# Optimization experiments

Hardware: AMD Instinct MI355X
Metric: run time of the kernel (lower is better)

## Reference

```python
import jax, jax.numpy as jnp
import numpy as np

NUM_HEADS = 16


def setup_inputs() -> dict:
    key = jax.random.key(0)
    ks = jax.random.split(key, 4)
    B, T, D, H3 = 8, 1024, 1024, 3072
    Hd = 1024
    sequence = jax.random.normal(ks[0], (B, T, D), dtype=jnp.float32)
    mask = jnp.ones((B, T), dtype=jnp.int32)
    qkv_w = jax.random.normal(ks[1], (D, H3), dtype=jnp.float32) * (1.0 / np.sqrt(D))
    qkv_b = jnp.zeros((H3,), dtype=jnp.float32)
    out_w = jax.random.normal(ks[2], (Hd, Hd), dtype=jnp.float32) * (1.0 / np.sqrt(Hd))
    out_b = jnp.zeros((Hd,), dtype=jnp.float32)
    return {"sequence": sequence, "mask": mask, "qkv_w": qkv_w, "qkv_b": qkv_b,
            "out_w": out_w, "out_b": out_b}


def reference(sequence, mask, qkv_w, qkv_b, out_w, out_b):
    B, T, D = sequence.shape
    H = NUM_HEADS
    hidden = out_w.shape[0]
    hd = hidden // H
    scale = hd ** -0.5

    # qkv projection -> (3, B, H, T, hd)
    qkv = (sequence @ qkv_w + qkv_b).reshape(B, T, 3, H, hd).transpose(2, 0, 3, 1, 4)
    Q, K, V = qkv[0], qkv[1], qkv[2]

    attn = jnp.einsum('bhqd,bhkd->bhqk', Q, K) * scale
    # torch: masked_fill where mask.unsqueeze(1).unsqueeze(-1) == 0  -> masks query rows
    attn = jnp.where(mask[:, None, :, None] == 0, -jnp.inf, attn)
    attn_weights = jax.nn.softmax(attn, axis=-1)

    # global NaN fallback: if any NaN, replace entire tensor with one-hot at k=0
    has_nan = jnp.any(jnp.isnan(attn_weights))
    fallback = jnp.zeros_like(attn_weights).at[:, :, :, 0].set(1.0)
    attn_weights = jnp.where(has_nan, fallback, attn_weights)
    # dropout is identity in eval / p=0.0

    out = jnp.einsum('bhqk,bhkd->bhqd', attn_weights, V)
    out = out.transpose(0, 2, 1, 3).reshape(B, T, hidden)
    out = out @ out_w + out_b
    return out, attn_weights
```

## Files before the change

### kernel.cpp

```cpp
#include <hip/hip_runtime.h>
#include <hip/hip_bf16.h>

using u16 = unsigned short;
typedef short bf16x8 __attribute__((ext_vector_type(8)));
typedef float f32x4 __attribute__((ext_vector_type(4)));

#define MFMA16(a, b, c) __builtin_amdgcn_mfma_f32_16x16x32_bf16((a), (b), (c), 0, 0, 0)

__device__ __forceinline__ float bf2f(u16 u) {
  union { unsigned int i; float f; } v; v.i = ((unsigned int)u) << 16; return v.f;
}
__device__ __forceinline__ u16 f2bf(float f) {
  __hip_bfloat16 h = __float2bfloat16(f);
  return *reinterpret_cast<u16*>(&h);
}
__device__ __forceinline__ void gld_lds16(const void* g, void* l) {
  __builtin_amdgcn_global_load_lds(
      (const __attribute__((address_space(1))) void*)g,
      (__attribute__((address_space(3))) void*)l, 16, 0, 0);
}

__global__ __launch_bounds__(256) void cvt_f32_bf16(
    const float* __restrict__ in, u16* __restrict__ out, int n8) {
  int i = blockIdx.x * 256 + threadIdx.x;
  if (i >= n8) return;
  f32x4 a = *(const f32x4*)&in[(size_t)i * 8];
  f32x4 b = *(const f32x4*)&in[(size_t)i * 8 + 4];
  bf16x8 o;
#pragma unroll
  for (int j = 0; j < 4; ++j) { o[j] = (short)f2bf(a[j]); o[4 + j] = (short)f2bf(b[j]); }
  *(bf16x8*)&out[(size_t)i * 8] = o;
}

__global__ __launch_bounds__(256) void transpose_cvt(
    const float* __restrict__ in, u16* __restrict__ out, int R, int C) {
  __shared__ float tile[32][33];
  int r0 = blockIdx.y * 32, c0 = blockIdx.x * 32;
  int tx = threadIdx.x, ty = threadIdx.y;
#pragma unroll
  for (int i = ty; i < 32; i += 8)
    tile[i][tx] = in[(size_t)(r0 + i) * C + c0 + tx];
  __syncthreads();
#pragma unroll
  for (int i = ty; i < 32; i += 8)
    out[(size_t)(c0 + i) * R + r0 + tx] = f2bf(tile[tx][i]);
}

#define TBM 128
#define TBN 128
#define TBK 64
#define SLD 136

__global__ __launch_bounds__(256) void qkv_gemm(
    const u16* __restrict__ A, const u16* __restrict__ Bt,
    const float* __restrict__ bias,
    u16* __restrict__ Qo, u16* __restrict__ Ko, u16* __restrict__ Vto) {
  const int K = 1024;
  __shared__ __align__(16) u16 LDSbuf[TBM * SLD];
  u16* Als = LDSbuf;
  u16* Bls = LDSbuf + TBM * TBK;
  int m0 = blockIdx.y * TBM, n0 = blockIdx.x * TBN;
  int tid = threadIdx.x;
  int w = tid >> 6, l = tid & 63, lr = l & 15, lg = l >> 4;
  int wm = w >> 1, wn = w & 1;

  f32x4 acc[4][4] = {};
  for (int k0 = 0; k0 < K; k0 += TBK) {
#pragma unroll
    for (int j = 0; j < 4; ++j) {
      int c = w * 4 + j;
      int e = c * 64 + l;
      int row = e >> 3, kq = (e & 7) * 8;
      gld_lds16(A + (size_t)(m0 + row) * K + k0 + kq, (char*)Als + (size_t)c * 1024);
      gld_lds16(Bt + (size_t)(n0 + row) * K + k0 + kq, (char*)Bls + (size_t)c * 1024);
    }
    __syncthreads();
#pragma unroll
    for (int ks = 0; ks < 2; ++ks) {
      bf16x8 a[4], b[4];
#pragma unroll
      for (int mt = 0; mt < 4; ++mt)
        a[mt] = *(const bf16x8*)&Als[(wm * 64 + mt * 16 + lr) * TBK + ks * 32 + lg * 8];
#pragma unroll
      for (int nt = 0; nt < 4; ++nt)
        b[nt] = *(const bf16x8*)&Bls[(wn * 64 + nt * 16 + lr) * TBK + ks * 32 + lg * 8];
#pragma unroll
      for (int mt = 0; mt < 4; ++mt)
#pragma unroll
        for (int nt = 0; nt < 4; ++nt)
          acc[mt][nt] = MFMA16(a[mt], b[nt], acc[mt][nt]);
    }
    __syncthreads();
  }

  int s = n0 >> 10;
#pragma unroll
  for (int mt = 0; mt < 4; ++mt)
#pragma unroll
    for (int nt = 0; nt < 4; ++nt) {
      int nl = wn * 64 + nt * 16 + lr;
      float bv = bias[n0 + nl];
#pragma unroll
      for (int r = 0; r < 4; ++r) {
        int ml = wm * 64 + mt * 16 + lg * 4 + r;
        u16 val = f2bf(acc[mt][nt][r] + bv);
        if (s == 2) LDSbuf[nl * SLD + ml] = val;
        else        LDSbuf[ml * SLD + nl] = val;
      }
    }
  __syncthreads();

  int b_ = m0 >> 10;
  int tbase = m0 & 1023;
#pragma unroll
  for (int c = 0; c < 8; ++c) {
    int idx = c * 256 + tid;
    int row = idx >> 4, colE = (idx & 15) * 8;
    bf16x8 v = *(const bf16x8*)&LDSbuf[row * SLD + colE];
    if (s == 2) {
      int rr = (n0 + row) & 1023;
      int h = rr >> 6, d = rr & 63;
      int bh = b_ * 16 + h;
      *(bf16x8*)&Vto[((size_t)bh * 64 + d) * 1024 + tbase + colE] = v;
    } else {
      int t = tbase + row;
      int rr = (n0 + colE) & 1023;
      int h = rr >> 6, d = rr & 63;
      int bh = b_ * 16 + h;
      u16* dst = (s == 0) ? Qo : Ko;
      *(bf16x8*)&dst[((size_t)bh * 1024 + t) * 64 + d] = v;
    }
  }
}

__global__ __launch_bounds__(256) void out_gemm(
    const u16* __restrict__ A, const u16* __restrict__ Bt,
    const float* __restrict__ bias, float* __restrict__ C) {
  const int K = 1024;
  __shared__ __align__(16) u16 Als[TBM * TBK];
  __shared__ __align__(16) u16 Bls[TBN * TBK];
  int m0 = blockIdx.y * TBM, n0 = blockIdx.x * TBN;
  int tid = threadIdx.x;
  int w = tid >> 6, l = tid & 63, lr = l & 15, lg = l >> 4;
  int wm = w >> 1, wn = w & 1;

  f32x4 acc[4][4] = {};
  for (int k0 = 0; k0 < K; k0 += TBK) {
#pragma unroll
    for (int j = 0; j < 4; ++j) {
      int c = w * 4 + j;
      int e = c * 64 + l;
      int row = e >> 3, kq = (e & 7) * 8;
      gld_lds16(A + (size_t)(m0 + row) * K + k0 + kq, (char*)Als + (size_t)c * 1024);
      gld_lds16(Bt + (size_t)(n0 + row) * K + k0 + kq, (char*)Bls + (size_t)c * 1024);
    }
    __syncthreads();
#pragma unroll
    for (int ks = 0; ks < 2; ++ks) {
      bf16x8 a[4], b[4];
#pragma unroll
      for (int mt = 0; mt < 4; ++mt)
        a[mt] = *(const bf16x8*)&Als[(wm * 64 + mt * 16 + lr) * TBK + ks * 32 + lg * 8];
#pragma unroll
      for (int nt = 0; nt < 4; ++nt)
        b[nt] = *(const bf16x8*)&Bls[(wn * 64 + nt * 16 + lr) * TBK + ks * 32 + lg * 8];
#pragma unroll
      for (int mt = 0; mt < 4; ++mt)
#pragma unroll
        for (int nt = 0; nt < 4; ++nt)
          acc[mt][nt] = MFMA16(a[mt], b[nt], acc[mt][nt]);
    }
    __syncthreads();
  }
#pragma unroll
  for (int mt = 0; mt < 4; ++mt)
#pragma unroll
    for (int nt = 0; nt < 4; ++nt) {
      int n = n0 + wn * 64 + nt * 16 + lr;
      float bv = bias[n];
#pragma unroll
      for (int r = 0; r < 4; ++r) {
        int m = m0 + wm * 64 + mt * 16 + lg * 4 + r;
        C[(size_t)m * 1024 + n] = acc[mt][nt][r] + bv;
      }
    }
}

#define QB 32
#define PLD 1032

__global__ __launch_bounds__(512) void attn_kernel(
    const u16* __restrict__ Q, const u16* __restrict__ K,
    const u16* __restrict__ Vt, float* __restrict__ Pout,
    u16* __restrict__ O) {
  __shared__ __align__(16) u16 Pls[QB * PLD];
  __shared__ __align__(16) u16 Qls[QB * 64];
  __shared__ float redM[8][QB];
  __shared__ float redS[8][QB];

  int bh = blockIdx.y;
  int q0 = blockIdx.x * QB;
  int tid = threadIdx.x;
  int w = tid >> 6, l = tid & 63, lr = l & 15, lg = l >> 4;
  const u16* Qp = Q + ((size_t)bh * 1024 + q0) * 64;
  const u16* Kp = K + (size_t)bh * 1024 * 64;
  const u16* Vp = Vt + (size_t)bh * 64 * 1024;

  if (tid < 256)
    *(bf16x8*)&Qls[tid * 8] = *(const bf16x8*)&Qp[tid * 8];
  __syncthreads();

  f32x4 sa[2][8] = {};
#pragma unroll
  for (int ks = 0; ks < 2; ++ks) {
    bf16x8 aq[2];
#pragma unroll
    for (int mt = 0; mt < 2; ++mt)
      aq[mt] = *(const bf16x8*)&Qls[(mt * 16 + lr) * 64 + ks * 32 + lg * 8];
#pragma unroll
    for (int n = 0; n < 8; ++n) {
      bf16x8 bk = *(const bf16x8*)&Kp[(size_t)(w * 128 + n * 16 + lr) * 64 + ks * 32 + lg * 8];
#pragma unroll
      for (int mt = 0; mt < 2; ++mt)
        sa[mt][n] = MFMA16(aq[mt], bk, sa[mt][n]);
    }
  }

  const float scale = 0.125f;
  float mx[2][4], sm[2][4];
#pragma unroll
  for (int mt = 0; mt < 2; ++mt)
#pragma unroll
    for (int r = 0; r < 4; ++r) {
      float m = -1e30f;
#pragma unroll
      for (int n = 0; n < 8; ++n) {
        sa[mt][n][r] *= scale;
        m = fmaxf(m, sa[mt][n][r]);
      }
#pragma unroll
      for (int off = 1; off < 16; off <<= 1) m = fmaxf(m, __shfl_xor(m, off));
      float s = 0.f;
#pragma unroll
      for (int n = 0; n < 8; ++n) {
        float p = __expf(sa[mt][n][r] - m);
        sa[mt][n][r] = p;
        s += p;
      }
#pragma unroll
      for (int off = 1; off < 16; off <<= 1) s += __shfl_xor(s, off);
      mx[mt][r] = m;
      sm[mt][r] = s;
    }
  if (lr == 0) {
#pragma unroll
    for (int mt = 0; mt < 2; ++mt)
#pragma unroll
      for (int r = 0; r < 4; ++r) {
        int row = mt * 16 + lg * 4 + r;
        redM[w][row] = mx[mt][r];
        redS[w][row] = sm[mt][r];
      }
  }
  __syncthreads();
#pragma unroll
  for (int mt = 0; mt < 2; ++mt)
#pragma unroll
    for (int r = 0; r < 4; ++r) {
      int row = mt * 16 + lg * 4 + r;
      float M = -1e30f;
#pragma unroll
      for (int w2 = 0; w2 < 8; ++w2) M = fmaxf(M, redM[w2][row]);
      float S = 0.f;
#pragma unroll
      for (int w2 = 0; w2 < 8; ++w2) S += redS[w2][row] * __expf(redM[w2][row] - M);
      float f = __expf(mx[mt][r] - M) / S;
#pragma unroll
      for (int n = 0; n < 8; ++n)
        Pls[row * PLD + w * 128 + n * 16 + lr] = f2bf(sa[mt][n][r] * f);
    }
  __syncthreads();

  size_t pb = ((size_t)bh * 1024 + q0) * 1024;
#pragma unroll
  for (int it = 0; it < 8; ++it) {
    int idx = it * 512 + tid;
    int row = idx >> 7, c8 = idx & 127;
    bf16x8 v = *(const bf16x8*)&Pls[row * PLD + c8 * 8];
    f32x4 a, b;
#pragma unroll
    for (int j = 0; j < 4; ++j) { a[j] = bf2f((u16)v[j]); b[j] = bf2f((u16)v[4 + j]); }
    size_t off = pb + (size_t)row * 1024 + c8 * 8;
    *(f32x4*)&Pout[off] = a;
    *(f32x4*)&Pout[off + 4] = b;
  }

  int wq = w >> 2, wd = w & 3;
  f32x4 oc = {};
#pragma unroll
  for (int kt = 0; kt < 32; ++kt) {
    bf16x8 ap = *(const bf16x8*)&Pls[(wq * 16 + lr) * PLD + kt * 32 + lg * 8];
    bf16x8 bv = *(const bf16x8*)&Vp[(size_t)(wd * 16 + lr) * 1024 + kt * 32 + lg * 8];
    oc = MFMA16(ap, bv, oc);
  }
  int b_ = bh >> 4, h = bh & 15;
#pragma unroll
  for (int r = 0; r < 4; ++r) {
    int q = q0 + wq * 16 + lg * 4 + r;
    O[((size_t)b_ * 1024 + q) * 1024 + h * 64 + wd * 16 + lr] = f2bf(oc[r]);
  }
}

extern "C" void kernel_launch(void* const* d_in, const int* in_sizes, int n_in,
                              void* d_out, int out_size, void* d_ws, size_t ws_size,
                              hipStream_t stream) {
  const float* seq   = (const float*)d_in[0];
  const float* qkv_w = (const float*)d_in[2];
  const float* qkv_b = (const float*)d_in[3];
  const float* out_w = (const float*)d_in[4];
  const float* out_b = (const float*)d_in[5];
  float* out = (float*)d_out;

  u16* seqb = (u16*)d_ws;
  u16* Qb   = seqb + 8388608;
  u16* Kb   = Qb + 8388608;
  u16* Vtb  = Kb + 8388608;
  u16* Ob   = Vtb + 8388608;
  u16* qkvT = Ob + 8388608;
  u16* owT  = qkvT + 3145728;

  cvt_f32_bf16<<<8388608 / (256 * 8), 256, 0, stream>>>(seq, seqb, 8388608 / 8);
  transpose_cvt<<<dim3(3072 / 32, 1024 / 32), dim3(32, 8), 0, stream>>>(qkv_w, qkvT, 1024, 3072);
  transpose_cvt<<<dim3(1024 / 32, 1024 / 32), dim3(32, 8), 0, stream>>>(out_w, owT, 1024, 1024);
  qkv_gemm<<<dim3(3072 / TBN, 8192 / TBM), 256, 0, stream>>>(seqb, qkvT, qkv_b, Qb, Kb, Vtb);
  attn_kernel<<<dim3(1024 / QB, 128), 512, 0, stream>>>(Qb, Kb, Vtb, out + 8388608, Ob);
  out_gemm<<<dim3(1024 / TBN, 8192 / TBM), 256, 0, stream>>>(Ob, owT, out_b, out);
}
```

Baseline: 428.6 us.

## Defer softmax normalization into PV accumulation and drop a block barrier

```diff
diff --git a/kernel.cpp b/kernel.cpp
--- a/kernel.cpp
+++ b/kernel.cpp
@@ -227,7 +227,6 @@
   }
 
   const float scale = 0.125f;
-  float mx[2][4], sm[2][4];
 #pragma unroll
   for (int mt = 0; mt < 2; ++mt)
 #pragma unroll
@@ -249,65 +248,78 @@
       }
 #pragma unroll
       for (int off = 1; off < 16; off <<= 1) s += __shfl_xor(s, off);
-      mx[mt][r] = m;
-      sm[mt][r] = s;
-    }
-  if (lr == 0) {
-#pragma unroll
-    for (int mt = 0; mt < 2; ++mt)
-#pragma unroll
-      for (int r = 0; r < 4; ++r) {
-        int row = mt * 16 + lg * 4 + r;
-        redM[w][row] = mx[mt][r];
-        redS[w][row] = sm[mt][r];
-      }
-  }
+      int row = mt * 16 + lg * 4 + r;
+      if (lr == 0) { redM[w][row] = m; redS[w][row] = s; }
+#pragma unroll
+      for (int n = 0; n < 8; ++n)
+        Pls[row * PLD + w * 128 + n * 16 + lr] = f2bf(sa[mt][n][r]);
+    }
   __syncthreads();
-#pragma unroll
-  for (int mt = 0; mt < 2; ++mt)
+
+  int wq = w >> 2, wd = w & 3;
+  float Mr[4], invSr[4];
+#pragma unroll
+  for (int r = 0; r < 4; ++r) {
+    int q = wq * 16 + lg * 4 + r;
+    float M = -1e30f;
+#pragma unroll
+    for (int w2 = 0; w2 < 8; ++w2) M = fmaxf(M, redM[w2][q]);
+    float S = 0.f;
+#pragma unroll
+    for (int w2 = 0; w2 < 8; ++w2) S += redS[w2][q] * __expf(redM[w2][q] - M);
+    Mr[r] = M;
+    invSr[r] = 1.f / S;
+  }
+  f32x4 oc = {};
+#pragma unroll
+  for (int w2 = 0; w2 < 8; ++w2) {
+    f32x4 os = {};
+#pragma unroll
+    for (int kt2 = 0; kt2 < 4; ++kt2) {
+      int kt = w2 * 4 + kt2;
+      bf16x8 ap = *(const bf16x8*)&Pls[(wq * 16 + lr) * PLD + kt * 32 + lg * 8];
+      bf16x8 bv = *(const bf16x8*)&Vp[(size_t)(wd * 16 + lr) * 1024 + kt * 32 + lg * 8];
+      os = MFMA16(ap, bv, os);
+    }
 #pragma unroll
     for (int r = 0; r < 4; ++r) {
-      int row = mt * 16 + lg * 4 + r;
-      float M = -1e30f;
-#pragma unroll
-      for (int w2 = 0; w2 < 8; ++w2) M = fmaxf(M, redM[w2][row]);
-      float S = 0.f;
-#pragma unroll
-      for (int w2 = 0; w2 < 8; ++w2) S += redS[w2][row] * __expf(redM[w2][row] - M);
-      float f = __expf(mx[mt][r] - M) / S;
-#pragma unroll
-      for (int n = 0; n < 8; ++n)
-        Pls[row * PLD + w * 128 + n * 16 + lr] = f2bf(sa[mt][n][r] * f);
-    }
-  __syncthreads();
-
-  size_t pb = ((size_t)bh * 1024 + q0) * 1024;
-#pragma unroll
-  for (int it = 0; it < 8; ++it) {
-    int idx = it * 512 + tid;
-    int row = idx >> 7, c8 = idx & 127;
-    bf16x8 v = *(const bf16x8*)&Pls[row * PLD + c8 * 8];
-    f32x4 a, b;
-#pragma unroll
-    for (int j = 0; j < 4; ++j) { a[j] = bf2f((u16)v[j]); b[j] = bf2f((u16)v[4 + j]); }
-    size_t off = pb + (size_t)row * 1024 + c8 * 8;
-    *(f32x4*)&Pout[off] = a;
-    *(f32x4*)&Pout[off + 4] = b;
-  }
-
-  int wq = w >> 2, wd = w & 3;
-  f32x4 oc = {};
-#pragma unroll
-  for (int kt = 0; kt < 32; ++kt) {
-    bf16x8 ap = *(const bf16x8*)&Pls[(wq * 16 + lr) * PLD + kt * 32 + lg * 8];
-    bf16x8 bv = *(const bf16x8*)&Vp[(size_t)(wd * 16 + lr) * 1024 + kt * 32 + lg * 8];
-    oc = MFMA16(ap, bv, oc);
+      int q = wq * 16 + lg * 4 + r;
+      oc[r] += os[r] * (__expf(redM[w2][q] - Mr[r]) * invSr[r]);
+    }
   }
   int b_ = bh >> 4, h = bh & 15;
 #pragma unroll
   for (int r = 0; r < 4; ++r) {
     int q = q0 + wq * 16 + lg * 4 + r;
     O[((size_t)b_ * 1024 + q) * 1024 + h * 64 + wd * 16 + lr] = f2bf(oc[r]);
+  }
+
+  {
+    int row = tid >> 4;
+    int cb = tid & 15;
+    float M = -1e30f;
+#pragma unroll
+    for (int w2 = 0; w2 < 8; ++w2) M = fmaxf(M, redM[w2][row]);
+    float S = 0.f;
+#pragma unroll
+    for (int w2 = 0; w2 < 8; ++w2) S += redS[w2][row] * __expf(redM[w2][row] - M);
+    float invS = 1.f / S;
+    size_t pb = ((size_t)bh * 1024 + q0 + row) * 1024;
+#pragma unroll
+    for (int it = 0; it < 8; ++it) {
+      float f = __expf(redM[it][row] - M) * invS;
+      int c8 = it * 16 + cb;
+      bf16x8 v = *(const bf16x8*)&Pls[row * PLD + c8 * 8];
+      f32x4 a, b;
+#pragma unroll
+      for (int j = 0; j < 4; ++j) {
+        a[j] = bf2f((u16)v[j]) * f;
+        b[j] = bf2f((u16)v[4 + j]) * f;
+      }
+      size_t off = pb + (size_t)c8 * 8;
+      __builtin_nontemporal_store(a, (f32x4*)&Pout[off]);
+      __builtin_nontemporal_store(b, (f32x4*)&Pout[off + 4]);
+    }
   }
 }
 
```

After: 368.5 us. 1.16x faster.
